# Performance work log

Hardware: AMD Instinct MI355X
Metric: run time of the kernel (lower is better)

## Reference

```python
import jax, jax.numpy as jnp
import numpy as np

N_NODES = 10000
N_EDGES = 640000
NODE_DIM = 128
EDGE_DIM = 32
OUT_DIM = 128


def setup_inputs() -> dict:
    key = jax.random.key(0)
    k_h, k_e, k_ef, k_w1, k_w2 = jax.random.split(key, 5)
    h = jax.random.normal(k_h, (N_NODES, NODE_DIM), dtype=jnp.float32)
    edge_index = jax.random.randint(k_e, (2, N_EDGES), 0, N_NODES, dtype=jnp.int64)
    edge_features = jax.random.normal(k_ef, (N_EDGES, EDGE_DIM), dtype=jnp.float32)
    in_dim = 2 * NODE_DIM + EDGE_DIM
    # Kaiming-ish init scale for realism
    W1 = jax.random.normal(k_w1, (in_dim, OUT_DIM), dtype=jnp.float32) / np.sqrt(in_dim)
    b1 = jnp.zeros((OUT_DIM,), dtype=jnp.float32)
    W2 = jax.random.normal(k_w2, (OUT_DIM, OUT_DIM), dtype=jnp.float32) / np.sqrt(OUT_DIM)
    b2 = jnp.zeros((OUT_DIM,), dtype=jnp.float32)
    return {"h": h, "edge_index": edge_index, "edge_features": edge_features,
            "n": N_NODES, "W1": W1, "b1": b1, "W2": W2, "b2": b2}


def reference(h, edge_index, edge_features, n, W1, b1, W2, b2):
    rows, cols = edge_index[0], edge_index[1]
    # gather source/target node features + edge features -> [E, 2*node_dim+edge_dim]
    msg_input = jnp.concatenate([h[rows], h[cols], edge_features], axis=-1)
    hidden = jax.nn.relu(msg_input @ W1 + b1)   # [E, out_dim]
    messages = hidden @ W2 + b2                 # [E, out_dim]
    # scatter-add messages onto destination rows -> [n, out_dim]
    out = jax.ops.segment_sum(messages, rows, num_segments=n)
    return out
```

## Files before the change

### kernel.cpp

```cpp
#include <hip/hip_runtime.h>
#include <hip/hip_bf16.h>


typedef __attribute__((ext_vector_type(8))) short bf16x8;
typedef __attribute__((ext_vector_type(4))) float f32x4;

#define ND 128
#define ED 32

__device__ __forceinline__ short f2bf(float x) {
  unsigned int u = __float_as_uint(x);
  unsigned int r = (u + 0x7FFFu + ((u >> 16) & 1u)) >> 16;
  return (short)r;
}

__device__ __forceinline__ float bf2f(short s) {
  return __uint_as_float(((unsigned int)(unsigned short)s) << 16);
}

__device__ __forceinline__ f32x4 bf8lo(bf16x8 v) {
  f32x4 r;
  #pragma unroll
  for (int j = 0; j < 4; ++j) r[j] = bf2f(v[j]);
  return r;
}
__device__ __forceinline__ f32x4 bf8hi(bf16x8 v) {
  f32x4 r;
  #pragma unroll
  for (int j = 0; j < 4; ++j) r[j] = bf2f(v[4 + j]);
  return r;
}

__device__ __forceinline__ int swz(int c) {
  int ct = c >> 4, cc = c & 15;
  return (ct >> 2) * 64 + (cc >> 2) * 16 + (ct & 3) * 4 + (cc & 3);
}

__global__ __launch_bounds__(256) void prep_kernel(
    const float* __restrict__ W1, const float* __restrict__ W2,
    const unsigned int* __restrict__ ei, short* __restrict__ w12t,
    short* __restrict__ w1eA, short* __restrict__ w2t, int* __restrict__ flag,
    int* __restrict__ counts, int N) {
  if (blockIdx.x == 0 && threadIdx.x == 0) {
    int is64 = 1;
    for (int i = 0; i < 16; ++i)
      if (ei[2 * i + 1] != 0u) is64 = 0;
    flag[0] = is64;
  }
  int t = blockIdx.x * blockDim.x + threadIdx.x;
  for (int i = t; i < N; i += 32768) counts[i] = 0;
  if (t < 256 * 128) {
    int np = t >> 7, k = t & 127;
    float v = (np < 128) ? W1[k * 128 + np] : W1[(128 + k) * 128 + (np - 128)];
    w12t[t] = f2bf(v);
  }
  if (t < 128 * 128) {
    int n = t >> 7, k = t & 127;
    w2t[t] = f2bf(W2[k * 128 + n]);
  }
  if (t < 8 * 64 * 8) {
    int ct = t >> 9, lane = (t >> 3) & 63, j = t & 7;
    int li = lane & 15, lg = lane >> 4;
    w1eA[t] = f2bf(W1[(256 + lg * 8 + j) * 128 + ct * 16 + li]);
  }
}

__global__ void hist_kernel(const void* __restrict__ ei, const int* __restrict__ flag,
                            int* __restrict__ counts, int* __restrict__ rank,
                            unsigned int* __restrict__ rc, int E) {
  int e = blockIdx.x * blockDim.x + threadIdx.x;
  if (e >= E) return;
  int f = flag[0];
  int r, c;
  if (f) {
    r = (int)((const long long*)ei)[e];
    c = (int)((const long long*)ei)[(long long)E + e];
  } else {
    r = ((const int*)ei)[e];
    c = ((const int*)ei)[E + e];
  }
  rank[e] = atomicAdd(&counts[r], 1);
  rc[e] = ((unsigned int)r << 16) | (unsigned int)c;
}

__global__ __launch_bounds__(1024) void scan_kernel(const int* __restrict__ counts,
                                                    int* __restrict__ row_ptr, int n) {
  __shared__ int wtot[16];
  int tid = threadIdx.x;
  int lane = tid & 63, w = tid >> 6;
  int base_i = tid * 16;
  int c[16];
  int tot = 0;
  #pragma unroll
  for (int j = 0; j < 16; ++j) {
    int i = base_i + j;
    c[j] = (i < n) ? counts[i] : 0;
    tot += c[j];
  }
  int x = tot;
  #pragma unroll
  for (int d = 1; d < 64; d <<= 1) {
    int t = __shfl_up(x, d);
    if (lane >= d) x += t;
  }
  if (lane == 63) wtot[w] = x;
  __syncthreads();
  if (w == 0) {
    int y = (lane < 16) ? wtot[lane] : 0;
    #pragma unroll
    for (int d = 1; d < 16; d <<= 1) {
      int t = __shfl_up(y, d);
      if (lane >= d) y += t;
    }
    if (lane < 16) wtot[lane] = y;
  }
  __syncthreads();
  int waveoff = (w == 0) ? 0 : wtot[w - 1];
  int run = waveoff + x - tot;
  if (tid == 0) row_ptr[0] = 0;
  #pragma unroll
  for (int j = 0; j < 16; ++j) {
    int i = base_i + j;
    if (i < n) {
      run += c[j];
      row_ptr[i + 1] = run;
    }
  }
}

__global__ __launch_bounds__(256, 4) void scatter_sg_kernel(
    const float* __restrict__ ef, const int* __restrict__ row_ptr,
    const int* __restrict__ rank, const unsigned int* __restrict__ rc,
    const float* __restrict__ h, const short* __restrict__ w12t,
    const float* __restrict__ b1, short* __restrict__ efb,
    int* __restrict__ ccol, float* __restrict__ s2, short* __restrict__ g2,
    int N, int E) {
  int b = blockIdx.x;
  int SGB = (N + 63) >> 6;
  if (b < SGB) {
    int lane = threadIdx.x & 63, w = threadIdx.x >> 6;
    int li = lane & 15, lg = lane >> 4;
    int base = b * 64 + w * 16;
    int rowm = base + li;
    if (rowm >= N) rowm = N - 1;
    float breg[8];
    #pragma unroll
    for (int nt = 0; nt < 8; ++nt) breg[nt] = b1[nt * 16 + li];
    f32x4 acc[16];
    #pragma unroll
    for (int nt = 0; nt < 16; ++nt) acc[nt] = (f32x4){0.f, 0.f, 0.f, 0.f};
    #pragma unroll
    for (int kc = 0; kc < 4; ++kc) {
      f32x4 f0 = *(const f32x4*)(h + (size_t)rowm * ND + kc * 32 + lg * 8);
      f32x4 f1 = *(const f32x4*)(h + (size_t)rowm * ND + kc * 32 + lg * 8 + 4);
      bf16x8 a;
      #pragma unroll
      for (int j = 0; j < 4; ++j) { a[j] = f2bf(f0[j]); a[4 + j] = f2bf(f1[j]); }
      #pragma unroll
      for (int nt = 0; nt < 16; ++nt) {
        bf16x8 bb = *(const bf16x8*)(w12t + (nt * 16 + li) * 128 + kc * 32 + lg * 8);
        acc[nt] = __builtin_amdgcn_mfma_f32_16x16x32_bf16(a, bb, acc[nt], 0, 0, 0);
      }
    }
    #pragma unroll
    for (int nt = 0; nt < 16; ++nt)
      #pragma unroll
      for (int r = 0; r < 4; ++r) {
        int row = base + lg * 4 + r;
        if (row < N) {
          if (nt < 8) {
            s2[(size_t)row * 128 + swz(nt * 16 + li)] = acc[nt][r] + breg[nt];
          } else {
            g2[(size_t)row * 128 + swz((nt - 8) * 16 + li)] = f2bf(acc[nt][r]);
          }
        }
      }
  } else {
    int gt = (b - SGB) * 256 + threadIdx.x;
    int e = gt >> 2, part = gt & 3;
    if (e < E) {
      unsigned int p = rc[e];
      int r = (int)(p >> 16), c = (int)(p & 0xffffu);
      int pos = row_ptr[r] + rank[e];
      f32x4 a0 = *(const f32x4*)(ef + (size_t)e * ED + part * 8);
      f32x4 a1 = *(const f32x4*)(ef + (size_t)e * ED + part * 8 + 4);
      bf16x8 ob;
      #pragma unroll
      for (int j = 0; j < 4; ++j) { ob[j] = f2bf(a0[j]); ob[4 + j] = f2bf(a1[j]); }
      *(bf16x8*)(efb + (size_t)pos * ED + part * 8) = ob;
      if (part == 0) ccol[pos] = c;
    }
  }
}

__global__ __launch_bounds__(128, 4) void layer1_kernel(
    const float* __restrict__ s2, const short* __restrict__ g2,
    const short* __restrict__ efb, const int* __restrict__ ccol,
    const short* __restrict__ w1eA, const int* __restrict__ row_ptr,
    float* __restrict__ hsum) {
  int node = blockIdx.x;
  int lane = threadIdx.x & 63;
  int w = threadIdx.x >> 6;
  int li = lane & 15, lg = lane >> 4;
  int rp = row_ptr[node], rpe = row_ptr[node + 1];
  int deg = rpe - rp;

  if (deg == 0) {
    if (li == 0) {
      #pragma unroll
      for (int nt = 0; nt < 4; ++nt)
        *(f32x4*)(hsum + (size_t)node * 128 + w * 64 + nt * 16 + lg * 4) =
            (f32x4){0.f, 0.f, 0.f, 0.f};
    }
    return;
  }

  bf16x8 wa[4];
  #pragma unroll
  for (int nt = 0; nt < 4; ++nt)
    wa[nt] = *(const bf16x8*)(w1eA + ((w * 4 + nt) * 64 + lane) * 8);
  f32x4 sreg[4];
  #pragma unroll
  for (int nt = 0; nt < 4; ++nt)
    sreg[nt] = *(const f32x4*)(s2 + (size_t)node * 128 + w * 64 + lg * 16 + nt * 4);
  f32x4 psum[4];
  #pragma unroll
  for (int nt = 0; nt < 4; ++nt) psum[nt] = (f32x4){0.f, 0.f, 0.f, 0.f};

  int ntiles = (deg + 15) >> 4;
  int last = rpe - 1;
  auto ldpos = [&](int t) {
    int p = rp + t * 16 + li;
    return p > last ? last : p;
  };

  int pA = ldpos(0), pB = ldpos(1);
  int cA = ccol[pA], cB = ccol[pB];
  bf16x8 eA = *(const bf16x8*)(efb + (size_t)pA * ED + lg * 8);
  bf16x8 eB = *(const bf16x8*)(efb + (size_t)pB * ED + lg * 8);
  const short* gpA = g2 + (size_t)cA * 128 + w * 64 + lg * 16;
  bf16x8 gA0 = *(const bf16x8*)gpA;
  bf16x8 gA1 = *(const bf16x8*)(gpA + 8);

  for (int t = 0; t < ntiles; ++t) {
    const short* gpB = g2 + (size_t)cB * 128 + w * 64 + lg * 16;
    bf16x8 gB0 = *(const bf16x8*)gpB;
    bf16x8 gB1 = *(const bf16x8*)(gpB + 8);
    int pC = ldpos(t + 2);
    int cC = ccol[pC];
    bf16x8 eC = *(const bf16x8*)(efb + (size_t)pC * ED + lg * 8);
    f32x4 a0 = __builtin_amdgcn_mfma_f32_16x16x32_bf16(wa[0], eA, (f32x4){0.f,0.f,0.f,0.f}, 0, 0, 0);
    f32x4 a1 = __builtin_amdgcn_mfma_f32_16x16x32_bf16(wa[1], eA, (f32x4){0.f,0.f,0.f,0.f}, 0, 0, 0);
    f32x4 a2 = __builtin_amdgcn_mfma_f32_16x16x32_bf16(wa[2], eA, (f32x4){0.f,0.f,0.f,0.f}, 0, 0, 0);
    f32x4 a3 = __builtin_amdgcn_mfma_f32_16x16x32_bf16(wa[3], eA, (f32x4){0.f,0.f,0.f,0.f}, 0, 0, 0);
    if ((t * 16 + li) < deg) {
      f32x4 v0 = a0 + sreg[0] + bf8lo(gA0);
      f32x4 v1 = a1 + sreg[1] + bf8hi(gA0);
      f32x4 v2 = a2 + sreg[2] + bf8lo(gA1);
      f32x4 v3 = a3 + sreg[3] + bf8hi(gA1);
      #pragma unroll
      for (int r = 0; r < 4; ++r) {
        psum[0][r] += (v0[r] > 0.f ? v0[r] : 0.f);
        psum[1][r] += (v1[r] > 0.f ? v1[r] : 0.f);
        psum[2][r] += (v2[r] > 0.f ? v2[r] : 0.f);
        psum[3][r] += (v3[r] > 0.f ? v3[r] : 0.f);
      }
    }
    cB = cC; eA = eB; eB = eC;
    gA0 = gB0; gA1 = gB1;
  }

  #pragma unroll
  for (int nt = 0; nt < 4; ++nt)
    #pragma unroll
    for (int r = 0; r < 4; ++r) {
      float v = psum[nt][r];
      v += __shfl_xor(v, 1);
      v += __shfl_xor(v, 2);
      v += __shfl_xor(v, 4);
      v += __shfl_xor(v, 8);
      psum[nt][r] = v;
    }
  if (li == 0) {
    #pragma unroll
    for (int nt = 0; nt < 4; ++nt)
      *(f32x4*)(hsum + (size_t)node * 128 + w * 64 + nt * 16 + lg * 4) = psum[nt];
  }
}

__global__ __launch_bounds__(256) void out_kernel(const float* __restrict__ hsum,
                                                  const short* __restrict__ w2t,
                                                  const float* __restrict__ b2,
                                                  const int* __restrict__ row_ptr,
                                                  float* __restrict__ out, int N) {
  int lane = threadIdx.x & 63, w = threadIdx.x >> 6;
  int li = lane & 15, lg = lane >> 4;
  int base = blockIdx.x * 64 + w * 16;
  int rowm = base + li;
  if (rowm >= N) rowm = N - 1;
  float breg[8];
  #pragma unroll
  for (int nt = 0; nt < 8; ++nt) breg[nt] = b2[nt * 16 + li];
  f32x4 acc[8];
  #pragma unroll
  for (int nt = 0; nt < 8; ++nt) acc[nt] = (f32x4){0.f, 0.f, 0.f, 0.f};
  #pragma unroll
  for (int kc = 0; kc < 4; ++kc) {
    f32x4 f0 = *(const f32x4*)(hsum + (size_t)rowm * 128 + kc * 32 + lg * 8);
    f32x4 f1 = *(const f32x4*)(hsum + (size_t)rowm * 128 + kc * 32 + lg * 8 + 4);
    bf16x8 a;
    #pragma unroll
    for (int j = 0; j < 4; ++j) { a[j] = f2bf(f0[j]); a[4 + j] = f2bf(f1[j]); }
    #pragma unroll
    for (int nt = 0; nt < 8; ++nt) {
      bf16x8 bb = *(const bf16x8*)(w2t + (nt * 16 + li) * 128 + kc * 32 + lg * 8);
      acc[nt] = __builtin_amdgcn_mfma_f32_16x16x32_bf16(a, bb, acc[nt], 0, 0, 0);
    }
  }
  #pragma unroll
  for (int r = 0; r < 4; ++r) {
    int row = base + lg * 4 + r;
    if (row < N) {
      float dg = (float)(row_ptr[row + 1] - row_ptr[row]);
      #pragma unroll
      for (int nt = 0; nt < 8; ++nt)
        out[(size_t)row * 128 + nt * 16 + li] = acc[nt][r] + dg * breg[nt];
    }
  }
}

extern "C" void kernel_launch(void* const* d_in, const int* in_sizes, int n_in,
                              void* d_out, int out_size, void* d_ws, size_t ws_size,
                              hipStream_t stream) {
  const float* h  = (const float*)d_in[0];
  const void*  ei = d_in[1];
  const float* ef = (const float*)d_in[2];
  const float* W1 = (const float*)d_in[4];
  const float* b1 = (const float*)d_in[5];
  const float* W2 = (const float*)d_in[6];
  const float* b2 = (const float*)d_in[7];
  float* out = (float*)d_out;
  int N = in_sizes[0] / ND;
  int E = in_sizes[2] / ED;

  char* ws = (char*)d_ws;
  size_t off = 0;
  auto alloc = [&](size_t bytes) {
    size_t o = off;
    off = (off + bytes + 255) & ~(size_t)255;
    return o;
  };
  int*          flag    = (int*)(ws + alloc(4));
  int*          counts  = (int*)(ws + alloc((size_t)N * 4));
  int*          row_ptr = (int*)(ws + alloc((size_t)(N + 1) * 4));
  int*          rank    = (int*)(ws + alloc((size_t)E * 4));
  unsigned int* rc      = (unsigned int*)(ws + alloc((size_t)E * 4));
  short*        w12t    = (short*)(ws + alloc(256 * 128 * 2));
  short*        w1eA    = (short*)(ws + alloc(8 * 64 * 8 * 2));
  short*        w2t     = (short*)(ws + alloc(128 * 128 * 2));
  float*        s2      = (float*)(ws + alloc((size_t)N * 128 * 4));
  short*        g2      = (short*)(ws + alloc((size_t)N * 128 * 2));
  float*        hsumb   = (float*)(ws + alloc((size_t)N * 128 * 4));
  short*        efb     = (short*)(ws + alloc((size_t)E * ED * 2));
  int*          ccol    = (int*)(ws + alloc((size_t)E * 4));

  int SGB = (N + 63) >> 6;
  int SCB = (4 * E + 255) >> 8;

  prep_kernel<<<128, 256, 0, stream>>>(W1, W2, (const unsigned int*)ei, w12t, w1eA, w2t,
                                       flag, counts, N);
  hist_kernel<<<(E + 255) / 256, 256, 0, stream>>>(ei, flag, counts, rank, rc, E);
  scan_kernel<<<1, 1024, 0, stream>>>(counts, row_ptr, N);
  scatter_sg_kernel<<<SGB + SCB, 256, 0, stream>>>(
      ef, row_ptr, rank, rc, h, w12t, b1, efb, ccol, s2, g2, N, E);
  layer1_kernel<<<N, 128, 0, stream>>>(s2, g2, efb, ccol, w1eA, row_ptr, hsumb);
  out_kernel<<<(N + 63) / 64, 256, 0, stream>>>(hsumb, w2t, b2, row_ptr, out, N);
}
```

Before: 134.1 us.

## Fuse prep with histogram and layer1 with output GEMV to cut launches

Merges the weight-prep and histogram kernels into one launch, with each histogram thread detecting int64 indices inline. The counts buffer is now zeroed by a memset instead of the prep kernel. The W2 projection is folded into the per-node layer1 kernel as a scalar fp32 GEMV over a shared-memory row, removing the hsum round trip and the separate MFMA out kernel. In exchange, each node block now reads all of W2 (32 KB) and does 16K scalar FMAs instead of using MFMA.

```diff
diff --git a/kernel.cpp b/kernel.cpp
--- a/kernel.cpp
+++ b/kernel.cpp
@@ -36,51 +36,49 @@
   return (ct >> 2) * 64 + (cc >> 2) * 16 + (ct & 3) * 4 + (cc & 3);
 }
 
-__global__ __launch_bounds__(256) void prep_kernel(
+__global__ __launch_bounds__(256) void prep_hist_kernel(
     const float* __restrict__ W1, const float* __restrict__ W2,
-    const unsigned int* __restrict__ ei, short* __restrict__ w12t,
-    short* __restrict__ w1eA, short* __restrict__ w2t, int* __restrict__ flag,
-    int* __restrict__ counts, int N) {
-  if (blockIdx.x == 0 && threadIdx.x == 0) {
-    int is64 = 1;
-    for (int i = 0; i < 16; ++i)
-      if (ei[2 * i + 1] != 0u) is64 = 0;
-    flag[0] = is64;
-  }
-  int t = blockIdx.x * blockDim.x + threadIdx.x;
-  for (int i = t; i < N; i += 32768) counts[i] = 0;
-  if (t < 256 * 128) {
-    int np = t >> 7, k = t & 127;
-    float v = (np < 128) ? W1[k * 128 + np] : W1[(128 + k) * 128 + (np - 128)];
-    w12t[t] = f2bf(v);
-  }
-  if (t < 128 * 128) {
-    int n = t >> 7, k = t & 127;
-    w2t[t] = f2bf(W2[k * 128 + n]);
-  }
-  if (t < 8 * 64 * 8) {
-    int ct = t >> 9, lane = (t >> 3) & 63, j = t & 7;
-    int li = lane & 15, lg = lane >> 4;
-    w1eA[t] = f2bf(W1[(256 + lg * 8 + j) * 128 + ct * 16 + li]);
-  }
-}
-
-__global__ void hist_kernel(const void* __restrict__ ei, const int* __restrict__ flag,
-                            int* __restrict__ counts, int* __restrict__ rank,
-                            unsigned int* __restrict__ rc, int E) {
-  int e = blockIdx.x * blockDim.x + threadIdx.x;
-  if (e >= E) return;
-  int f = flag[0];
-  int r, c;
-  if (f) {
-    r = (int)((const long long*)ei)[e];
-    c = (int)((const long long*)ei)[(long long)E + e];
+    const void* __restrict__ ei, int* __restrict__ counts,
+    int* __restrict__ rank, unsigned int* __restrict__ rc,
+    short* __restrict__ w12t, short* __restrict__ w1eA, short* __restrict__ w2t,
+    int E) {
+  int b = blockIdx.x;
+  if (b < 128) {
+    int t = b * 256 + threadIdx.x;
+    if (t < 256 * 128) {
+      int np = t >> 7, k = t & 127;
+      float v = (np < 128) ? W1[k * 128 + np] : W1[(128 + k) * 128 + (np - 128)];
+      w12t[t] = f2bf(v);
+    }
+    if (t < 128 * 128) {
+      int n = t >> 7, k = t & 127;
+      w2t[t] = f2bf(W2[k * 128 + n]);
+    }
+    if (t < 8 * 64 * 8) {
+      int ct = t >> 9, lane = (t >> 3) & 63, j = t & 7;
+      int li = lane & 15, lg = lane >> 4;
+      w1eA[t] = f2bf(W1[(256 + lg * 8 + j) * 128 + ct * 16 + li]);
+    }
   } else {
-    r = ((const int*)ei)[e];
-    c = ((const int*)ei)[E + e];
-  }
-  rank[e] = atomicAdd(&counts[r], 1);
-  rc[e] = ((unsigned int)r << 16) | (unsigned int)c;
+    int e = (b - 128) * 256 + threadIdx.x;
+    if (e < E) {
+      const unsigned int* u = (const unsigned int*)ei;
+      int is64 = 1;
+      #pragma unroll
+      for (int i = 0; i < 16; ++i)
+        if (u[2 * i + 1] != 0u) is64 = 0;
+      int r, c;
+      if (is64) {
+        r = (int)((const long long*)ei)[e];
+        c = (int)((const long long*)ei)[(long long)E + e];
+      } else {
+        r = ((const int*)ei)[e];
+        c = ((const int*)ei)[E + e];
+      }
+      rank[e] = atomicAdd(&counts[r], 1);
+      rc[e] = ((unsigned int)r << 16) | (unsigned int)c;
+    }
+  }
 }
 
 __global__ __launch_bounds__(1024) void scan_kernel(const int* __restrict__ counts,
@@ -193,25 +191,23 @@
   }
 }
 
-__global__ __launch_bounds__(128, 4) void layer1_kernel(
+__global__ __launch_bounds__(128, 4) void layer1out_kernel(
     const float* __restrict__ s2, const short* __restrict__ g2,
     const short* __restrict__ efb, const int* __restrict__ ccol,
-    const short* __restrict__ w1eA, const int* __restrict__ row_ptr,
-    float* __restrict__ hsum) {
+    const short* __restrict__ w1eA, const short* __restrict__ w2t,
+    const float* __restrict__ b2, const int* __restrict__ row_ptr,
+    float* __restrict__ out) {
+  __shared__ float hs[128];
   int node = blockIdx.x;
-  int lane = threadIdx.x & 63;
-  int w = threadIdx.x >> 6;
+  int tid = threadIdx.x;
+  int lane = tid & 63;
+  int w = tid >> 6;
   int li = lane & 15, lg = lane >> 4;
   int rp = row_ptr[node], rpe = row_ptr[node + 1];
   int deg = rpe - rp;
 
   if (deg == 0) {
-    if (li == 0) {
-      #pragma unroll
-      for (int nt = 0; nt < 4; ++nt)
-        *(f32x4*)(hsum + (size_t)node * 128 + w * 64 + nt * 16 + lg * 4) =
-            (f32x4){0.f, 0.f, 0.f, 0.f};
-    }
+    out[(size_t)node * 128 + tid] = 0.f;
     return;
   }
 
@@ -284,49 +280,20 @@
   if (li == 0) {
     #pragma unroll
     for (int nt = 0; nt < 4; ++nt)
-      *(f32x4*)(hsum + (size_t)node * 128 + w * 64 + nt * 16 + lg * 4) = psum[nt];
-  }
-}
-
-__global__ __launch_bounds__(256) void out_kernel(const float* __restrict__ hsum,
-                                                  const short* __restrict__ w2t,
-                                                  const float* __restrict__ b2,
-                                                  const int* __restrict__ row_ptr,
-                                                  float* __restrict__ out, int N) {
-  int lane = threadIdx.x & 63, w = threadIdx.x >> 6;
-  int li = lane & 15, lg = lane >> 4;
-  int base = blockIdx.x * 64 + w * 16;
-  int rowm = base + li;
-  if (rowm >= N) rowm = N - 1;
-  float breg[8];
-  #pragma unroll
-  for (int nt = 0; nt < 8; ++nt) breg[nt] = b2[nt * 16 + li];
-  f32x4 acc[8];
-  #pragma unroll
-  for (int nt = 0; nt < 8; ++nt) acc[nt] = (f32x4){0.f, 0.f, 0.f, 0.f};
-  #pragma unroll
-  for (int kc = 0; kc < 4; ++kc) {
-    f32x4 f0 = *(const f32x4*)(hsum + (size_t)rowm * 128 + kc * 32 + lg * 8);
-    f32x4 f1 = *(const f32x4*)(hsum + (size_t)rowm * 128 + kc * 32 + lg * 8 + 4);
-    bf16x8 a;
-    #pragma unroll
-    for (int j = 0; j < 4; ++j) { a[j] = f2bf(f0[j]); a[4 + j] = f2bf(f1[j]); }
-    #pragma unroll
-    for (int nt = 0; nt < 8; ++nt) {
-      bf16x8 bb = *(const bf16x8*)(w2t + (nt * 16 + li) * 128 + kc * 32 + lg * 8);
-      acc[nt] = __builtin_amdgcn_mfma_f32_16x16x32_bf16(a, bb, acc[nt], 0, 0, 0);
-    }
-  }
-  #pragma unroll
-  for (int r = 0; r < 4; ++r) {
-    int row = base + lg * 4 + r;
-    if (row < N) {
-      float dg = (float)(row_ptr[row + 1] - row_ptr[row]);
-      #pragma unroll
-      for (int nt = 0; nt < 8; ++nt)
-        out[(size_t)row * 128 + nt * 16 + li] = acc[nt][r] + dg * breg[nt];
-    }
-  }
+      *(f32x4*)(hs + w * 64 + nt * 16 + lg * 4) = psum[nt];
+  }
+  __syncthreads();
+
+  const short* wcol = w2t + tid * 128;
+  float acc = 0.f;
+  #pragma unroll
+  for (int kc = 0; kc < 16; ++kc) {
+    bf16x8 wv = *(const bf16x8*)(wcol + kc * 8);
+    const float* hp = hs + kc * 8;
+    #pragma unroll
+    for (int j = 0; j < 8; ++j) acc = fmaf(hp[j], bf2f(wv[j]), acc);
+  }
+  out[(size_t)node * 128 + tid] = acc + (float)deg * b2[tid];
 }
 
 extern "C" void kernel_launch(void* const* d_in, const int* in_sizes, int n_in,
@@ -350,7 +317,6 @@
     off = (off + bytes + 255) & ~(size_t)255;
     return o;
   };
-  int*          flag    = (int*)(ws + alloc(4));
   int*          counts  = (int*)(ws + alloc((size_t)N * 4));
   int*          row_ptr = (int*)(ws + alloc((size_t)(N + 1) * 4));
   int*          rank    = (int*)(ws + alloc((size_t)E * 4));
@@ -360,19 +326,17 @@
   short*        w2t     = (short*)(ws + alloc(128 * 128 * 2));
   float*        s2      = (float*)(ws + alloc((size_t)N * 128 * 4));
   short*        g2      = (short*)(ws + alloc((size_t)N * 128 * 2));
-  float*        hsumb   = (float*)(ws + alloc((size_t)N * 128 * 4));
   short*        efb     = (short*)(ws + alloc((size_t)E * ED * 2));
   int*          ccol    = (int*)(ws + alloc((size_t)E * 4));
 
   int SGB = (N + 63) >> 6;
   int SCB = (4 * E + 255) >> 8;
 
-  prep_kernel<<<128, 256, 0, stream>>>(W1, W2, (const unsigned int*)ei, w12t, w1eA, w2t,
-                                       flag, counts, N);
-  hist_kernel<<<(E + 255) / 256, 256, 0, stream>>>(ei, flag, counts, rank, rc, E);
+  hipMemsetAsync(counts, 0, (size_t)N * 4, stream);
+  prep_hist_kernel<<<128 + (E + 255) / 256, 256, 0, stream>>>(
+      W1, W2, ei, counts, rank, rc, w12t, w1eA, w2t, E);
   scan_kernel<<<1, 1024, 0, stream>>>(counts, row_ptr, N);
   scatter_sg_kernel<<<SGB + SCB, 256, 0, stream>>>(
       ef, row_ptr, rank, rc, h, w12t, b1, efb, ccol, s2, g2, N, E);
-  layer1_kernel<<<N, 128, 0, stream>>>(s2, g2, efb, ccol, w1eA, row_ptr, hsumb);
-  out_kernel<<<(N + 63) / 64, 256, 0, stream>>>(hsumb, w2t, b2, row_ptr, out, N);
-}
+  layer1out_kernel<<<N, 128, 0, stream>>>(s2, g2, efb, ccol, w1eA, w2t, b2, row_ptr, out);
+}
```

Result: slower. 162.6 us (+21.3%).

## Merge prep and histogram kernels, make layer1 a persistent grid-stride kernel

Applied to the files above, without the earlier changes.

Weight conversion and edge histogram now run in one launch, with a memset zeroing the counts and every edge thread detecting the index dtype itself instead of reading a flag. The layer1 kernel switches from one block per node to a fixed grid of 2048 blocks that stride over nodes, so each block loads the W1 edge-weight fragments once. The aim is fewer launches and less per-block setup. In exchange, every edge thread repeats 16 dtype-check loads, and the static node assignment can leave load imbalance on high-degree nodes.

```diff
diff --git a/kernel.cpp b/kernel.cpp
--- a/kernel.cpp
+++ b/kernel.cpp
@@ -7,6 +7,7 @@
 
 #define ND 128
 #define ED 32
+#define NL1 2048
 
 __device__ __forceinline__ short f2bf(float x) {
   unsigned int u = __float_as_uint(x);
@@ -36,51 +37,49 @@
   return (ct >> 2) * 64 + (cc >> 2) * 16 + (ct & 3) * 4 + (cc & 3);
 }
 
-__global__ __launch_bounds__(256) void prep_kernel(
+__global__ __launch_bounds__(256) void prep_hist_kernel(
     const float* __restrict__ W1, const float* __restrict__ W2,
-    const unsigned int* __restrict__ ei, short* __restrict__ w12t,
-    short* __restrict__ w1eA, short* __restrict__ w2t, int* __restrict__ flag,
-    int* __restrict__ counts, int N) {
-  if (blockIdx.x == 0 && threadIdx.x == 0) {
-    int is64 = 1;
-    for (int i = 0; i < 16; ++i)
-      if (ei[2 * i + 1] != 0u) is64 = 0;
-    flag[0] = is64;
-  }
-  int t = blockIdx.x * blockDim.x + threadIdx.x;
-  for (int i = t; i < N; i += 32768) counts[i] = 0;
-  if (t < 256 * 128) {
-    int np = t >> 7, k = t & 127;
-    float v = (np < 128) ? W1[k * 128 + np] : W1[(128 + k) * 128 + (np - 128)];
-    w12t[t] = f2bf(v);
-  }
-  if (t < 128 * 128) {
-    int n = t >> 7, k = t & 127;
-    w2t[t] = f2bf(W2[k * 128 + n]);
-  }
-  if (t < 8 * 64 * 8) {
-    int ct = t >> 9, lane = (t >> 3) & 63, j = t & 7;
-    int li = lane & 15, lg = lane >> 4;
-    w1eA[t] = f2bf(W1[(256 + lg * 8 + j) * 128 + ct * 16 + li]);
-  }
-}
-
-__global__ void hist_kernel(const void* __restrict__ ei, const int* __restrict__ flag,
-                            int* __restrict__ counts, int* __restrict__ rank,
-                            unsigned int* __restrict__ rc, int E) {
-  int e = blockIdx.x * blockDim.x + threadIdx.x;
-  if (e >= E) return;
-  int f = flag[0];
-  int r, c;
-  if (f) {
-    r = (int)((const long long*)ei)[e];
-    c = (int)((const long long*)ei)[(long long)E + e];
+    const void* __restrict__ ei, int* __restrict__ counts,
+    int* __restrict__ rank, unsigned int* __restrict__ rc,
+    short* __restrict__ w12t, short* __restrict__ w1eA, short* __restrict__ w2t,
+    int E) {
+  int b = blockIdx.x;
+  if (b < 128) {
+    int t = b * 256 + threadIdx.x;
+    if (t < 256 * 128) {
+      int np = t >> 7, k = t & 127;
+      float v = (np < 128) ? W1[k * 128 + np] : W1[(128 + k) * 128 + (np - 128)];
+      w12t[t] = f2bf(v);
+    }
+    if (t < 128 * 128) {
+      int n = t >> 7, k = t & 127;
+      w2t[t] = f2bf(W2[k * 128 + n]);
+    }
+    if (t < 8 * 64 * 8) {
+      int ct = t >> 9, lane = (t >> 3) & 63, j = t & 7;
+      int li = lane & 15, lg = lane >> 4;
+      w1eA[t] = f2bf(W1[(256 + lg * 8 + j) * 128 + ct * 16 + li]);
+    }
   } else {
-    r = ((const int*)ei)[e];
-    c = ((const int*)ei)[E + e];
-  }
-  rank[e] = atomicAdd(&counts[r], 1);
-  rc[e] = ((unsigned int)r << 16) | (unsigned int)c;
+    int e = (b - 128) * 256 + threadIdx.x;
+    if (e < E) {
+      const unsigned int* u = (const unsigned int*)ei;
+      int is64 = 1;
+      #pragma unroll
+      for (int i = 0; i < 16; ++i)
+        if (u[2 * i + 1] != 0u) is64 = 0;
+      int r, c;
+      if (is64) {
+        r = (int)((const long long*)ei)[e];
+        c = (int)((const long long*)ei)[(long long)E + e];
+      } else {
+        r = ((const int*)ei)[e];
+        c = ((const int*)ei)[E + e];
+      }
+      rank[e] = atomicAdd(&counts[r], 1);
+      rc[e] = ((unsigned int)r << 16) | (unsigned int)c;
+    }
+  }
 }
 
 __global__ __launch_bounds__(1024) void scan_kernel(const int* __restrict__ counts,
@@ -197,94 +196,97 @@
     const float* __restrict__ s2, const short* __restrict__ g2,
     const short* __restrict__ efb, const int* __restrict__ ccol,
     const short* __restrict__ w1eA, const int* __restrict__ row_ptr,
-    float* __restrict__ hsum) {
-  int node = blockIdx.x;
+    float* __restrict__ hsum, int N) {
   int lane = threadIdx.x & 63;
   int w = threadIdx.x >> 6;
   int li = lane & 15, lg = lane >> 4;
-  int rp = row_ptr[node], rpe = row_ptr[node + 1];
-  int deg = rpe - rp;
-
-  if (deg == 0) {
-    if (li == 0) {
-      #pragma unroll
-      for (int nt = 0; nt < 4; ++nt)
-        *(f32x4*)(hsum + (size_t)node * 128 + w * 64 + nt * 16 + lg * 4) =
-            (f32x4){0.f, 0.f, 0.f, 0.f};
-    }
-    return;
-  }
 
   bf16x8 wa[4];
   #pragma unroll
   for (int nt = 0; nt < 4; ++nt)
     wa[nt] = *(const bf16x8*)(w1eA + ((w * 4 + nt) * 64 + lane) * 8);
-  f32x4 sreg[4];
-  #pragma unroll
-  for (int nt = 0; nt < 4; ++nt)
-    sreg[nt] = *(const f32x4*)(s2 + (size_t)node * 128 + w * 64 + lg * 16 + nt * 4);
-  f32x4 psum[4];
-  #pragma unroll
-  for (int nt = 0; nt < 4; ++nt) psum[nt] = (f32x4){0.f, 0.f, 0.f, 0.f};
-
-  int ntiles = (deg + 15) >> 4;
-  int last = rpe - 1;
-  auto ldpos = [&](int t) {
-    int p = rp + t * 16 + li;
-    return p > last ? last : p;
-  };
-
-  int pA = ldpos(0), pB = ldpos(1);
-  int cA = ccol[pA], cB = ccol[pB];
-  bf16x8 eA = *(const bf16x8*)(efb + (size_t)pA * ED + lg * 8);
-  bf16x8 eB = *(const bf16x8*)(efb + (size_t)pB * ED + lg * 8);
-  const short* gpA = g2 + (size_t)cA * 128 + w * 64 + lg * 16;
-  bf16x8 gA0 = *(const bf16x8*)gpA;
-  bf16x8 gA1 = *(const bf16x8*)(gpA + 8);
-
-  for (int t = 0; t < ntiles; ++t) {
-    const short* gpB = g2 + (size_t)cB * 128 + w * 64 + lg * 16;
-    bf16x8 gB0 = *(const bf16x8*)gpB;
-    bf16x8 gB1 = *(const bf16x8*)(gpB + 8);
-    int pC = ldpos(t + 2);
-    int cC = ccol[pC];
-    bf16x8 eC = *(const bf16x8*)(efb + (size_t)pC * ED + lg * 8);
-    f32x4 a0 = __builtin_amdgcn_mfma_f32_16x16x32_bf16(wa[0], eA, (f32x4){0.f,0.f,0.f,0.f}, 0, 0, 0);
-    f32x4 a1 = __builtin_amdgcn_mfma_f32_16x16x32_bf16(wa[1], eA, (f32x4){0.f,0.f,0.f,0.f}, 0, 0, 0);
-    f32x4 a2 = __builtin_amdgcn_mfma_f32_16x16x32_bf16(wa[2], eA, (f32x4){0.f,0.f,0.f,0.f}, 0, 0, 0);
-    f32x4 a3 = __builtin_amdgcn_mfma_f32_16x16x32_bf16(wa[3], eA, (f32x4){0.f,0.f,0.f,0.f}, 0, 0, 0);
-    if ((t * 16 + li) < deg) {
-      f32x4 v0 = a0 + sreg[0] + bf8lo(gA0);
-      f32x4 v1 = a1 + sreg[1] + bf8hi(gA0);
-      f32x4 v2 = a2 + sreg[2] + bf8lo(gA1);
-      f32x4 v3 = a3 + sreg[3] + bf8hi(gA1);
+
+  for (int node = blockIdx.x; node < N; node += NL1) {
+    int rp = row_ptr[node], rpe = row_ptr[node + 1];
+    int deg = rpe - rp;
+
+    if (deg == 0) {
+      if (li == 0) {
+        #pragma unroll
+        for (int nt = 0; nt < 4; ++nt)
+          *(f32x4*)(hsum + (size_t)node * 128 + w * 64 + nt * 16 + lg * 4) =
+              (f32x4){0.f, 0.f, 0.f, 0.f};
+      }
+      continue;
+    }
+
+    f32x4 sreg[4];
+    #pragma unroll
+    for (int nt = 0; nt < 4; ++nt)
+      sreg[nt] = *(const f32x4*)(s2 + (size_t)node * 128 + w * 64 + lg * 16 + nt * 4);
+    f32x4 psum[4];
+    #pragma unroll
+    for (int nt = 0; nt < 4; ++nt) psum[nt] = (f32x4){0.f, 0.f, 0.f, 0.f};
+
+    int ntiles = (deg + 15) >> 4;
+    int last = rpe - 1;
+    auto ldpos = [&](int t) {
+      int p = rp + t * 16 + li;
+      return p > last ? last : p;
+    };
+
+    int pA = ldpos(0), pB = ldpos(1);
+    int cA = ccol[pA], cB = ccol[pB];
+    bf16x8 eA = *(const bf16x8*)(efb + (size_t)pA * ED + lg * 8);
+    bf16x8 eB = *(const bf16x8*)(efb + (size_t)pB * ED + lg * 8);
+    const short* gpA = g2 + (size_t)cA * 128 + w * 64 + lg * 16;
+    bf16x8 gA0 = *(const bf16x8*)gpA;
+    bf16x8 gA1 = *(const bf16x8*)(gpA + 8);
+
+    for (int t = 0; t < ntiles; ++t) {
+      const short* gpB = g2 + (size_t)cB * 128 + w * 64 + lg * 16;
+      bf16x8 gB0 = *(const bf16x8*)gpB;
+      bf16x8 gB1 = *(const bf16x8*)(gpB + 8);
+      int pC = ldpos(t + 2);
+      int cC = ccol[pC];
+      bf16x8 eC = *(const bf16x8*)(efb + (size_t)pC * ED + lg * 8);
+      f32x4 a0 = __builtin_amdgcn_mfma_f32_16x16x32_bf16(wa[0], eA, (f32x4){0.f,0.f,0.f,0.f}, 0, 0, 0);
+      f32x4 a1 = __builtin_amdgcn_mfma_f32_16x16x32_bf16(wa[1], eA, (f32x4){0.f,0.f,0.f,0.f}, 0, 0, 0);
+      f32x4 a2 = __builtin_amdgcn_mfma_f32_16x16x32_bf16(wa[2], eA, (f32x4){0.f,0.f,0.f,0.f}, 0, 0, 0);
+      f32x4 a3 = __builtin_amdgcn_mfma_f32_16x16x32_bf16(wa[3], eA, (f32x4){0.f,0.f,0.f,0.f}, 0, 0, 0);
+      if ((t * 16 + li) < deg) {
+        f32x4 v0 = a0 + sreg[0] + bf8lo(gA0);
+        f32x4 v1 = a1 + sreg[1] + bf8hi(gA0);
+        f32x4 v2 = a2 + sreg[2] + bf8lo(gA1);
+        f32x4 v3 = a3 + sreg[3] + bf8hi(gA1);
+        #pragma unroll
+        for (int r = 0; r < 4; ++r) {
+          psum[0][r] += (v0[r] > 0.f ? v0[r] : 0.f);
+          psum[1][r] += (v1[r] > 0.f ? v1[r] : 0.f);
+          psum[2][r] += (v2[r] > 0.f ? v2[r] : 0.f);
+          psum[3][r] += (v3[r] > 0.f ? v3[r] : 0.f);
+        }
+      }
+      cB = cC; eA = eB; eB = eC;
+      gA0 = gB0; gA1 = gB1;
+    }
+
+    #pragma unroll
+    for (int nt = 0; nt < 4; ++nt)
       #pragma unroll
       for (int r = 0; r < 4; ++r) {
-        psum[0][r] += (v0[r] > 0.f ? v0[r] : 0.f);
-        psum[1][r] += (v1[r] > 0.f ? v1[r] : 0.f);
-        psum[2][r] += (v2[r] > 0.f ? v2[r] : 0.f);
-        psum[3][r] += (v3[r] > 0.f ? v3[r] : 0.f);
-      }
-    }
-    cB = cC; eA = eB; eB = eC;
-    gA0 = gB0; gA1 = gB1;
-  }
-
-  #pragma unroll
-  for (int nt = 0; nt < 4; ++nt)
-    #pragma unroll
-    for (int r = 0; r < 4; ++r) {
-      float v = psum[nt][r];
-      v += __shfl_xor(v, 1);
-      v += __shfl_xor(v, 2);
-      v += __shfl_xor(v, 4);
-      v += __shfl_xor(v, 8);
-      psum[nt][r] = v;
-    }
-  if (li == 0) {
-    #pragma unroll
-    for (int nt = 0; nt < 4; ++nt)
-      *(f32x4*)(hsum + (size_t)node * 128 + w * 64 + nt * 16 + lg * 4) = psum[nt];
+        float v = psum[nt][r];
+        v += __shfl_xor(v, 1);
+        v += __shfl_xor(v, 2);
+        v += __shfl_xor(v, 4);
+        v += __shfl_xor(v, 8);
+        psum[nt][r] = v;
+      }
+    if (li == 0) {
+      #pragma unroll
+      for (int nt = 0; nt < 4; ++nt)
+        *(f32x4*)(hsum + (size_t)node * 128 + w * 64 + nt * 16 + lg * 4) = psum[nt];
+    }
   }
 }
 
@@ -350,7 +352,6 @@
     off = (off + bytes + 255) & ~(size_t)255;
     return o;
   };
-  int*          flag    = (int*)(ws + alloc(4));
   int*          counts  = (int*)(ws + alloc((size_t)N * 4));
   int*          row_ptr = (int*)(ws + alloc((size_t)(N + 1) * 4));
   int*          rank    = (int*)(ws + alloc((size_t)E * 4));
@@ -367,12 +368,12 @@
   int SGB = (N + 63) >> 6;
   int SCB = (4 * E + 255) >> 8;
 
-  prep_kernel<<<128, 256, 0, stream>>>(W1, W2, (const unsigned int*)ei, w12t, w1eA, w2t,
-                                       flag, counts, N);
-  hist_kernel<<<(E + 255) / 256, 256, 0, stream>>>(ei, flag, counts, rank, rc, E);
+  hipMemsetAsync(counts, 0, (size_t)N * 4, stream);
+  prep_hist_kernel<<<128 + (E + 255) / 256, 256, 0, stream>>>(
+      W1, W2, ei, counts, rank, rc, w12t, w1eA, w2t, E);
   scan_kernel<<<1, 1024, 0, stream>>>(counts, row_ptr, N);
   scatter_sg_kernel<<<SGB + SCB, 256, 0, stream>>>(
       ef, row_ptr, rank, rc, h, w12t, b1, efb, ccol, s2, g2, N, E);
-  layer1_kernel<<<N, 128, 0, stream>>>(s2, g2, efb, ccol, w1eA, row_ptr, hsumb);
+  layer1_kernel<<<NL1, 128, 0, stream>>>(s2, g2, efb, ccol, w1eA, row_ptr, hsumb, N);
   out_kernel<<<(N + 63) / 64, 256, 0, stream>>>(hsumb, w2t, b2, row_ptr, out, N);
 }
```

Result: no change. 133.8 us (median of 2 runs) (-0.2%).
